# Kernel tuning notes

Hardware: AMD Instinct MI355X
Metric: run time of the kernel (lower is better)

## Reference

```python
import jax, jax.numpy as jnp
import numpy as np

MARGIN = 1.0
B, D, NUM_CLASSES = 8192, 128, 10


def setup_inputs() -> dict:
    key = jax.random.key(0)
    k1, k2 = jax.random.split(key)
    embeddings = jax.random.normal(k1, (B, D), dtype=jnp.float32)
    labels = jax.random.randint(k2, (B,), 0, NUM_CLASSES, dtype=jnp.int64)
    return {"embeddings": embeddings, "labels": labels}


def reference(embeddings, labels):
    # pairwise Euclidean distances d[i, j] = sqrt(sum((e_i - e_j)^2))
    sq = jnp.sum(embeddings * embeddings, axis=-1)               # [B]
    d2 = sq[:, None] + sq[None, :] - 2.0 * (embeddings @ embeddings.T)
    dist = jnp.sqrt(jnp.maximum(d2, 0.0))                        # [B, B]

    same = labels[:, None] == labels[None, :]                    # [B, B] bool
    neg_inf = jnp.float32(-jnp.inf)
    pos_inf = jnp.float32(jnp.inf)

    # hardest positive: max distance among same-class (includes self, dist 0, harmless)
    hardest_pos = jnp.max(jnp.where(same, dist, neg_inf), axis=1)   # [B]
    # hardest negative: min distance among different-class
    hardest_neg = jnp.min(jnp.where(same, pos_inf, dist), axis=1)   # [B]

    per_anchor = jax.nn.relu(hardest_pos - hardest_neg + MARGIN)    # [B]
    # use_gt_than_zero_mean=False -> divide by batch size
    return jnp.sum(per_anchor) / per_anchor.shape[0]
```

## Files before the change

### kernel.cpp

```cpp
#include <hip/hip_runtime.h>
#include <hip/hip_bf16.h>
#include <cstdint>

#define BATCH 8192
#define DIM   128
#define KBYTES 192
#define MARGIN 1.0f
#define SEPI   193548
#define SCALE  16.0f
#define INVS2  (1.0f / 256.0f)

typedef __attribute__((ext_vector_type(4))) int   int4v;
typedef __attribute__((ext_vector_type(4))) float f32x4;

__device__ __forceinline__ void async_copy16(const void* g, void* lds) {
    __builtin_amdgcn_global_load_lds(
        (const __attribute__((address_space(1))) unsigned int*)g,
        (__attribute__((address_space(3))) unsigned int*)lds, 16, 0, 0);
}

__global__ __launch_bounds__(256) void bhtl_prep(
    const float* __restrict__ emb,
    const int* __restrict__ labels,
    signed char* __restrict__ EA,
    signed char* __restrict__ EB,
    int* __restrict__ sq,
    unsigned* __restrict__ hp2,
    unsigned* __restrict__ hn2)
{
    const int hw  = threadIdx.x >> 5;
    const int l   = threadIdx.x & 31;
    const int row = blockIdx.x * 8 + hw;
    const float4 e = ((const float4*)(emb + (size_t)row * DIM))[l];

    int a0 = (int)rintf(e.x * SCALE); a0 = min(127, max(-127, a0));
    int a1 = (int)rintf(e.y * SCALE); a1 = min(127, max(-127, a1));
    int a2 = (int)rintf(e.z * SCALE); a2 = min(127, max(-127, a2));
    int a3 = (int)rintf(e.w * SCALE); a3 = min(127, max(-127, a3));
    unsigned pa = (a0 & 255) | ((a1 & 255) << 8) | ((a2 & 255) << 16) | ((a3 & 255) << 24);
    *(unsigned*)(EA + (size_t)row * KBYTES + l * 4) = pa;
    *(unsigned*)(EB + (size_t)row * KBYTES + l * 4) = pa;

    if (l < 16) {
        const int lab = labels[row];
        unsigned wa = 0, wb = 0;
        #pragma unroll
        for (int b = 0; b < 4; ++b) {
            int j = l * 4 + b;
            int in = (j < 60) && (j / 6 == lab);
            wa |= (unsigned)((in ?  127 : 0) & 255) << (8 * b);
            wb |= (unsigned)((in ? -127 : 0) & 255) << (8 * b);
        }
        *(unsigned*)(EA + (size_t)row * KBYTES + 128 + l * 4) = wa;
        *(unsigned*)(EB + (size_t)row * KBYTES + 128 + l * 4) = wb;
    }

    int s = a0 * a0 + a1 * a1 + a2 * a2 + a3 * a3;
    #pragma unroll
    for (int d = 1; d < 32; d <<= 1) s += __shfl_xor(s, d, 64);
    if (l == 0) {
        sq[row]  = s;
        hp2[row] = 0u;
        hn2[row] = 0x7F800000u;
    }
}

__global__ __launch_bounds__(64) void bhtl_main(
    const signed char* __restrict__ EA,
    const signed char* __restrict__ EB,
    const int* __restrict__ sq,
    unsigned* __restrict__ hp2,
    unsigned* __restrict__ hn2)
{
    __shared__ __align__(16) unsigned char B_s[3][3072];
    __shared__ __align__(16) int sqm[256];

    const int lane = threadIdx.x;
    const int q    = lane >> 4;
    const int ln   = lane & 15;
    const int rb   = blockIdx.x >> 5;
    const int js   = blockIdx.x & 31;
    const int rowbase = rb * 64;
    const int jbase   = js * 256;

    int4v af[4][3];
    #pragma unroll
    for (int m = 0; m < 4; ++m)
        #pragma unroll
        for (int kc = 0; kc < 3; ++kc) {
            af[m][kc] = *(const int4v*)(
                EA + (size_t)(rowbase + m * 16 + ln) * KBYTES + kc * 64 + q * 16);
            asm("" : "+v"(af[m][kc]));
        }

    async_copy16(sq + jbase + lane * 4, &sqm[0]);

    asm volatile("s_waitcnt vmcnt(0)" ::: "memory");

    auto stageB = [&](int buf, int ch) {
        const int jb = jbase + ch * 16;
        #pragma unroll
        for (int c = 0; c < 3; ++c) {
            int U   = c * 64 + lane;
            int col = U / 12;
            int u   = U - col * 12;
            int g   = (u < 8) ? (u ^ (col & 7)) : (8 + ((u - 8) ^ (col & 3)));
            async_copy16(EB + (size_t)(jb + col) * KBYTES + g * 16,
                         &B_s[buf][c * 1024]);
        }
    };

    int mp[4] = {INT_MIN, INT_MIN, INT_MIN, INT_MIN};
    int mn[4] = {INT_MAX, INT_MAX, INT_MAX, INT_MAX};

    auto doIter = [&](int ch, int buf, bool doStage, int stageBuf, bool last) {
        if (last) asm volatile("s_waitcnt vmcnt(0)" ::: "memory");
        else      asm volatile("s_waitcnt vmcnt(3)" ::: "memory");

        int4v bfr[3];
        #pragma unroll
        for (int kc = 0; kc < 3; ++kc) {
            const int t    = kc * 4 + q;
            const int unit = (t < 8) ? (t ^ (ln & 7)) : (8 + (q ^ (ln & 3)));
            bfr[kc] = *(const int4v*)(&B_s[buf][(ln * 12 + unit) * 16]);
        }
        int4v sqj = *(const int4v*)(&sqm[ch * 16 + q * 4]);

        if (doStage) stageB(stageBuf, ch + 2);

        int4v acc[4];
        const int4v zero = {0, 0, 0, 0};
        #pragma unroll
        for (int m = 0; m < 4; ++m) acc[m] = zero;
        #pragma unroll
        for (int kc = 0; kc < 3; ++kc)
            #pragma unroll
            for (int m = 0; m < 4; ++m)
                acc[m] = __builtin_amdgcn_mfma_i32_16x16x64_i8(
                    bfr[kc], af[m][kc], acc[m], 0, 0, 0);

        #pragma unroll
        for (int m = 0; m < 4; ++m)
            #pragma unroll
            for (int r = 0; r < 4; ++r) {
                int val = sqj[r] - 2 * acc[m][r];
                mp[m] = max(mp[m], val);
                mn[m] = min(mn[m], val);
            }
    };

    stageB(0, 0);
    stageB(1, 1);

    #pragma unroll 1
    for (int base = 0; base < 15; base += 3) {
        doIter(base,     0, true,      2, false);
        doIter(base + 1, 1, true,      0, false);
        doIter(base + 2, 2, base < 12, 1, false);
    }
    doIter(15, 0, false, 0, true);

    #pragma unroll
    for (int m = 0; m < 4; ++m) {
        int a = mp[m], b = mn[m];
        a = max(a, __shfl_xor(a, 16, 64));
        a = max(a, __shfl_xor(a, 32, 64));
        b = min(b, __shfl_xor(b, 16, 64));
        b = min(b, __shfl_xor(b, 32, 64));
        if (q == 0) {
            const int row = rowbase + m * 16 + ln;
            const int sqi = sq[row];
            float hpf = fmaxf((float)(sqi + a - SEPI) * INVS2, 0.0f);
            float hnf = fmaxf((float)(sqi + b) * INVS2, 0.0f);
            atomicMax(&hp2[row], __float_as_uint(hpf));
            atomicMin(&hn2[row], __float_as_uint(hnf));
        }
    }
}

__global__ __launch_bounds__(1024) void bhtl_final(
    const unsigned* __restrict__ hp2,
    const unsigned* __restrict__ hn2,
    float* __restrict__ out)
{
    __shared__ float red[16];
    float sum = 0.f;
    for (int i = threadIdx.x; i < BATCH; i += 1024) {
        float hp = sqrtf(__uint_as_float(hp2[i]));
        float hn = sqrtf(__uint_as_float(hn2[i]));
        sum += fmaxf(hp - hn + MARGIN, 0.f);
    }
    #pragma unroll
    for (int d = 1; d < 64; d <<= 1) sum += __shfl_xor(sum, d, 64);
    int wv = threadIdx.x >> 6;
    if ((threadIdx.x & 63) == 0) red[wv] = sum;
    __syncthreads();
    if (threadIdx.x < 64) {
        float v = (threadIdx.x < 16) ? red[threadIdx.x] : 0.f;
        #pragma unroll
        for (int d = 1; d < 16; d <<= 1) v += __shfl_xor(v, d, 64);
        if (threadIdx.x == 0) out[0] = v / (float)BATCH;
    }
}

extern "C" void kernel_launch(void* const* d_in, const int* in_sizes, int n_in,
                              void* d_out, int out_size, void* d_ws, size_t ws_size,
                              hipStream_t stream)
{
    const float* emb    = (const float*)d_in[0];
    const int*   labels = (const int*)d_in[1];
    float*       out    = (float*)d_out;

    char* ws = (char*)d_ws;
    signed char* EA  = (signed char*)ws;
    signed char* EB  = (signed char*)(ws + 2 * 1024 * 1024);
    int*      sq   = (int*)     (ws + 4 * 1024 * 1024);
    unsigned* hp2  = (unsigned*)(ws + 4 * 1024 * 1024 + 32 * 1024);
    unsigned* hn2  = (unsigned*)(ws + 4 * 1024 * 1024 + 64 * 1024);

    bhtl_prep<<<BATCH / 8, 256, 0, stream>>>(emb, labels, EA, EB, sq, hp2, hn2);
    bhtl_main<<<4096, 64, 0, stream>>>(EA, EB, sq, hp2, hn2);
    bhtl_final<<<1, 1024, 0, stream>>>(hp2, hn2, out);
}
```

Before: 85.52 us.

## Exploit distance matrix symmetry by computing only upper-triangular tile blocks

The grid now covers only upper-triangular 256x256 tile pairs (528 instead of 1024), so each block also reduces column-wise max/min through cross-lane shuffles into shared memory. Those column results are then atomically merged into the per-anchor hardest positive and negative for the column rows. This roughly halves the int8 MFMA work. In exchange it adds per-iteration shuffle reductions, extra atomics, and a serial loop to decode the triangular block index. A possible concern is that colMax and colMin are written and then read back by different lanes without a barrier between them. With a single 64-thread wavefront this may still work in practice.

Result: slower. 106.3 us (+24.3%).

```diff
diff --git a/kernel.cpp b/kernel.cpp
--- a/kernel.cpp
+++ b/kernel.cpp
@@ -74,14 +74,20 @@
 {
     __shared__ __align__(16) unsigned char B_s[3][3072];
     __shared__ __align__(16) int sqm[256];
+    __shared__ int colMax[256];
+    __shared__ int colMin[256];
 
     const int lane = threadIdx.x;
     const int q    = lane >> 4;
     const int ln   = lane & 15;
-    const int rb   = blockIdx.x >> 5;
-    const int js   = blockIdx.x & 31;
-    const int rowbase = rb * 64;
-    const int jbase   = js * 256;
+
+    int t = blockIdx.x >> 2;
+    const int s = blockIdx.x & 3;
+    int I = 0;
+    while (t >= 32 - I) { t -= 32 - I; ++I; }
+    const int J = I + t;
+    const int rowbase = I * 256 + s * 64;
+    const int jbase   = J * 256;
 
     int4v af[4][3];
     #pragma unroll
@@ -92,6 +98,11 @@
                 EA + (size_t)(rowbase + m * 16 + ln) * KBYTES + kc * 64 + q * 16);
             asm("" : "+v"(af[m][kc]));
         }
+
+    int sqa[4];
+    #pragma unroll
+    for (int m = 0; m < 4; ++m)
+        sqa[m] = sq[rowbase + m * 16 + ln];
 
     async_copy16(sq + jbase + lane * 4, &sqm[0]);
 
@@ -120,8 +131,8 @@
         int4v bfr[3];
         #pragma unroll
         for (int kc = 0; kc < 3; ++kc) {
-            const int t    = kc * 4 + q;
-            const int unit = (t < 8) ? (t ^ (ln & 7)) : (8 + (q ^ (ln & 3)));
+            const int t2   = kc * 4 + q;
+            const int unit = (t2 < 8) ? (t2 ^ (ln & 7)) : (8 + (q ^ (ln & 3)));
             bfr[kc] = *(const int4v*)(&B_s[buf][(ln * 12 + unit) * 16]);
         }
         int4v sqj = *(const int4v*)(&sqm[ch * 16 + q * 4]);
@@ -147,6 +158,25 @@
                 mp[m] = max(mp[m], val);
                 mn[m] = min(mn[m], val);
             }
+
+        #pragma unroll
+        for (int r = 0; r < 4; ++r) {
+            int v0 = sqa[0] - 2 * acc[0][r];
+            int v1 = sqa[1] - 2 * acc[1][r];
+            int v2 = sqa[2] - 2 * acc[2][r];
+            int v3 = sqa[3] - 2 * acc[3][r];
+            int cx = max(max(v0, v1), max(v2, v3));
+            int cn = min(min(v0, v1), min(v2, v3));
+            #pragma unroll
+            for (int d = 1; d < 16; d <<= 1) {
+                cx = max(cx, __shfl_xor(cx, d, 64));
+                cn = min(cn, __shfl_xor(cn, d, 64));
+            }
+            if (ln == 0) {
+                colMax[ch * 16 + q * 4 + r] = cx;
+                colMin[ch * 16 + q * 4 + r] = cn;
+            }
+        }
     };
 
     stageB(0, 0);
@@ -169,12 +199,23 @@
         b = min(b, __shfl_xor(b, 32, 64));
         if (q == 0) {
             const int row = rowbase + m * 16 + ln;
-            const int sqi = sq[row];
-            float hpf = fmaxf((float)(sqi + a - SEPI) * INVS2, 0.0f);
-            float hnf = fmaxf((float)(sqi + b) * INVS2, 0.0f);
+            float hpf = fmaxf((float)(sqa[m] + a - SEPI) * INVS2, 0.0f);
+            float hnf = fmaxf((float)(sqa[m] + b) * INVS2, 0.0f);
             atomicMax(&hp2[row], __float_as_uint(hpf));
             atomicMin(&hn2[row], __float_as_uint(hnf));
         }
+    }
+
+    #pragma unroll
+    for (int c4 = 0; c4 < 4; ++c4) {
+        const int col = c4 * 64 + lane;
+        const int cx  = colMax[col];
+        const int cn  = colMin[col];
+        const int sqc = sqm[col];
+        float hpf = fmaxf((float)(sqc + cx - SEPI) * INVS2, 0.0f);
+        float hnf = fmaxf((float)(sqc + cn) * INVS2, 0.0f);
+        atomicMax(&hp2[jbase + col], __float_as_uint(hpf));
+        atomicMin(&hn2[jbase + col], __float_as_uint(hnf));
     }
 }
 
@@ -219,6 +260,6 @@
     unsigned* hn2  = (unsigned*)(ws + 4 * 1024 * 1024 + 64 * 1024);
 
     bhtl_prep<<<BATCH / 8, 256, 0, stream>>>(emb, labels, EA, EB, sq, hp2, hn2);
-    bhtl_main<<<4096, 64, 0, stream>>>(EA, EB, sq, hp2, hn2);
+    bhtl_main<<<528 * 4, 64, 0, stream>>>(EA, EB, sq, hp2, hn2);
     bhtl_final<<<1, 1024, 0, stream>>>(hp2, hn2, out);
 }
```
